# Optimization experiments

Measured on AMD Instinct MI355X. Metric: run time of the kernel, lower is better.

The kernel has to match this reference:

```python
import jax, jax.numpy as jnp
import numpy as np

EMB = 512
GP = 128
NH = 8
HD = EMB // NH  # 64
B = 2
S = 1024


def _rel_shift(x):
    # Faithful port of DoubleAttentionLayer._rel_shift (pads dim 1, reinterprets
    # (B, J+1, K, n) as (J+1, B, K, n), drops first slice). Row-major reshape
    # semantics match torch .view on contiguous tensors exactly.
    Bsz, J, K, N = x.shape
    zp = jnp.zeros((Bsz, 1, K, N), x.dtype)
    xp = jnp.concatenate([zp, x], axis=1).reshape(J + 1, Bsz, K, N)
    return xp[1:].reshape(Bsz, J, K, N)


def _layernorm(x):
    # nn.LayerNorm(emb_dim, elementwise_affine=False), eps=1e-5
    m = jnp.mean(x, axis=-1, keepdims=True)
    v = jnp.var(x, axis=-1, keepdims=True)
    return (x - m) / jnp.sqrt(v + 1e-5)


def _attention(q, k, v, Bc, Bp, gpe, mask, Wp_w, Wp_b):
    Bsz, J, E = q.shape
    K = k.shape[1]
    # content scores
    qc = jnp.tanh((q + Bc).reshape(Bsz, J, NH, HD))
    kh = jnp.tanh(k.reshape(Bsz, K, NH, HD))
    ctx = jnp.einsum('bjnd,bknd->bjkn', qc, kh)
    # position scores (tanh before reshape in source for qp -- elementwise, same math)
    qp = jnp.tanh(q + Bp).reshape(Bsz, J, NH, HD)
    kp = jnp.tanh((gpe @ Wp_w + Wp_b).reshape(Bsz, -1, NH, HD))
    pos = jnp.einsum('bjnd,bknd->bjkn', qp, kp)
    pad = ctx.shape[2] - pos.shape[2]  # static; 0 in this configuration
    if pad > 0:
        # replicate-pad pos at front of k dim; constant(0)-pad mask (torch F.pad defaults)
        pos = jnp.concatenate([jnp.broadcast_to(pos[:, :, :1], (Bsz, J, pad, NH)), pos], axis=2)
        mask = jnp.concatenate([jnp.zeros(mask.shape[:2] + (pad, mask.shape[3]), mask.dtype), mask], axis=2)
    pos = _rel_shift(pos)
    att = (ctx + pos) / (HD ** 0.5) - 1e30 * mask
    att = jax.nn.softmax(att, axis=2)
    vh = jnp.tanh(v.reshape(Bsz, K, NH, HD))
    return jnp.einsum('bjkn,bknd->bjnd', att, vh).reshape(Bsz, J, E)


def setup_inputs() -> dict:
    key = jax.random.key(0)
    ks = jax.random.split(key, 12)
    u_emb = jax.random.normal(ks[0], (B, S, EMB), jnp.float32)
    f_emb = jax.random.normal(ks[1], (B, S, EMB), jnp.float32)
    gpe = jax.random.normal(ks[2], (B, S, GP), jnp.float32)
    # causal masks: 1 where attention is disallowed, broadcast over heads
    causal = (1.0 - jnp.tril(jnp.ones((S, S), jnp.float32)))[None, :, :, None]
    u_mask = jnp.broadcast_to(causal, (B, S, S, 1))
    f_mask = jnp.broadcast_to(causal, (B, S, S, 1))
    w = 0.02
    Wq_w = w * jax.random.normal(ks[3], (EMB, EMB), jnp.float32)
    Wq_b = jnp.zeros((EMB,), jnp.float32)
    Wkv_w = w * jax.random.normal(ks[4], (EMB, 2 * EMB), jnp.float32)
    Wkv_b = jnp.zeros((2 * EMB,), jnp.float32)
    Wp_w = w * jax.random.normal(ks[5], (GP, EMB), jnp.float32)
    Wp_b = jnp.zeros((EMB,), jnp.float32)
    Wu_w = w * jax.random.normal(ks[6], (EMB, EMB), jnp.float32)
    Wu_b = jnp.zeros((EMB,), jnp.float32)
    Bfc = 0.2 * jax.random.normal(ks[7], (1, 1, EMB), jnp.float32)
    Bfp = 0.2 * jax.random.normal(ks[8], (1, 1, EMB), jnp.float32)
    Buc = 0.2 * jax.random.normal(ks[9], (1, 1, EMB), jnp.float32)
    Bup = 0.2 * jax.random.normal(ks[10], (1, 1, EMB), jnp.float32)
    return {"u_emb": u_emb, "f_emb": f_emb, "gpe": gpe, "u_mask": u_mask, "f_mask": f_mask,
            "Wq_w": Wq_w, "Wq_b": Wq_b, "Wkv_w": Wkv_w, "Wkv_b": Wkv_b,
            "Wp_w": Wp_w, "Wp_b": Wp_b, "Wu_w": Wu_w, "Wu_b": Wu_b,
            "Bfc": Bfc, "Bfp": Bfp, "Buc": Buc, "Bup": Bup}


def reference(u_emb, f_emb, gpe, u_mask, f_mask, Wq_w, Wq_b, Wkv_w, Wkv_b,
              Wp_w, Wp_b, Wu_w, Wu_b, Bfc, Bfp, Buc, Bup):
    # first_part=True path: f_mem = f_emb (memory buffer registration has no output effect)
    q_u = f_emb @ Wu_w + Wu_b
    kv = f_emb @ Wkv_w + Wkv_b
    k, v = jnp.split(kv, 2, axis=-1)
    u_out = _layernorm(u_emb + _attention(q_u, k, v, Buc, Bup, gpe, u_mask, Wp_w, Wp_b))
    # last_layer=False: second attention over f stream
    q_f = f_emb @ Wq_w + Wq_b
    f_out = _layernorm(f_emb + _attention(q_f, k, v, Bfc, Bfp, gpe, f_mask, Wp_w, Wp_b))
    return (u_out, f_out)
```

## Files before the change

kernel.cpp:

```cpp
#include <hip/hip_runtime.h>
#include <math.h>

#define EMB 512
#define NH 8
#define HD 64
#define BB 2
#define SS 1024
#define ROWS (BB * SS)

typedef __attribute__((ext_vector_type(8))) short bhalf8;
typedef __attribute__((ext_vector_type(4))) float f32x4;
typedef __attribute__((ext_vector_type(8))) unsigned short us8;
typedef unsigned short ushort_t;

typedef const __attribute__((address_space(1))) void gas_void;
typedef __attribute__((address_space(3))) void las_void;

__device__ __forceinline__ void gl2lds16(const void* g, void* l) {
  __builtin_amdgcn_global_load_lds((gas_void*)g, (las_void*)l, 16, 0, 0);
}

__device__ __forceinline__ unsigned short f2bf(float x) {
  unsigned u = __float_as_uint(x);
  u = (u + 0x7FFFu + ((u >> 16) & 1u)) >> 16;
  return (unsigned short)u;
}
__device__ __forceinline__ float bf2f(unsigned short v) {
  return __uint_as_float(((unsigned)v) << 16);
}
__device__ __forceinline__ float fast_tanh(float x) {
  x = fminf(15.f, fmaxf(-15.f, x));
  const float e = __expf(2.f * x);
  return (e - 1.f) / (e + 1.f);
}

__global__ __launch_bounds__(256) void prep_kernel(
    const float* __restrict__ f_emb, const float* __restrict__ gpe,
    const float* __restrict__ Wu, const float* __restrict__ Wq,
    const float* __restrict__ Wkv, const float* __restrict__ Wp,
    ushort_t* __restrict__ fembB, ushort_t* __restrict__ gpeB,
    ushort_t* __restrict__ WuT, ushort_t* __restrict__ WqT,
    ushort_t* __restrict__ WkvT, ushort_t* __restrict__ WpT,
    ushort_t* __restrict__ Qcomb) {
  __shared__ __align__(16) ushort_t sT[64 * 72];
  const int bid = blockIdx.x;
  const int tid = threadIdx.x;

  if (bid < 160) {
    const bool isF = bid < 128;
    const float* src = isF ? f_emb : gpe;
    ushort_t* dst = isF ? fembB : gpeB;
    const size_t base = (size_t)(isF ? bid : bid - 128) * 8192;
#pragma unroll
    for (int j = 0; j < 4; ++j) {
      const size_t off = base + ((size_t)j * 256 + tid) * 8;
      const float4 a = *(const float4*)&src[off];
      const float4 b = *(const float4*)&src[off + 4];
      us8 o;
      o[0] = f2bf(a.x); o[1] = f2bf(a.y); o[2] = f2bf(a.z); o[3] = f2bf(a.w);
      o[4] = f2bf(b.x); o[5] = f2bf(b.y); o[6] = f2bf(b.z); o[7] = f2bf(b.w);
      *(us8*)&dst[off] = o;
    }
  } else if (bid < 432) {
    int t = bid - 160;
    const float* W;
    ushort_t* WT;
    int Nw, Kd, k0, n0;
    if (t < 64) {
      W = Wu; WT = WuT; Nw = 512; Kd = 512;
      k0 = (t >> 3) * 64; n0 = (t & 7) * 64;
    } else if (t < 128) {
      t -= 64; W = Wq; WT = WqT; Nw = 512; Kd = 512;
      k0 = (t >> 3) * 64; n0 = (t & 7) * 64;
    } else if (t < 256) {
      t -= 128; W = Wkv; WT = WkvT; Nw = 1024; Kd = 512;
      k0 = (t >> 4) * 64; n0 = (t & 15) * 64;
    } else {
      t -= 256; W = Wp; WT = WpT; Nw = 512; Kd = 128;
      k0 = (t >> 3) * 64; n0 = (t & 7) * 64;
    }
    const int kk = tid >> 2, seg = tid & 3;
    const float* src = &W[(size_t)(k0 + kk) * Nw + n0 + seg * 16];
    float v[16];
    *(float4*)&v[0] = *(const float4*)&src[0];
    *(float4*)&v[4] = *(const float4*)&src[4];
    *(float4*)&v[8] = *(const float4*)&src[8];
    *(float4*)&v[12] = *(const float4*)&src[12];
#pragma unroll
    for (int i = 0; i < 16; ++i) sT[(seg * 16 + i) * 72 + kk] = f2bf(v[i]);
    __syncthreads();
#pragma unroll
    for (int p = 0; p < 2; ++p) {
      const int idx = p * 256 + tid;
      const int n = idx >> 3, c8 = (idx & 7) * 8;
      const us8 o = *(const us8*)&sT[n * 72 + c8];
      *(us8*)&WT[(size_t)(n0 + n) * Kd + k0 + c8] = o;
    }
  } else {
    const int t2 = tid >> 7, rem = tid & 127;
    const int h = rem >> 4, d4 = (rem & 15) * 4;
    *(ushort4*)&Qcomb[((size_t)t2 * ROWS + 1023) * 1024 + h * 128 + 64 + d4] =
        make_ushort4(0, 0, 0, 0);
  }
}

__global__ __launch_bounds__(256, 3) void projpe_kernel(
    const ushort_t* __restrict__ fembB, const ushort_t* __restrict__ gpeB,
    const ushort_t* __restrict__ WuT, const ushort_t* __restrict__ WqT,
    const ushort_t* __restrict__ WkvT, const ushort_t* __restrict__ WpT,
    const float* __restrict__ Wu_b, const float* __restrict__ Wq_b,
    const float* __restrict__ Wkv_b, const float* __restrict__ Wp_b,
    const float* __restrict__ Buc, const float* __restrict__ Bup,
    const float* __restrict__ Bfc, const float* __restrict__ Bfp,
    ushort_t* __restrict__ Qcomb, ushort_t* __restrict__ Kcomb,
    ushort_t* __restrict__ vhT) {
  const int bx = blockIdx.x;
  const int mb = blockIdx.y * 128;
  const int tid = threadIdx.x;
  const int w = tid >> 6, lane = tid & 63;
  const int ln = lane & 15, quad = lane >> 4;
  const int wm = (w >> 1) * 64, wn = (w & 1) * 32;

  __shared__ __align__(16) ushort_t sMem[24576];

  const bool isPe = (bx >= 32);
  const int nb = isPe ? 0 : bx * 64;
  const int npbase = isPe ? (bx - 32) * 64 : 0;
  const ushort_t* Asrc = isPe ? gpeB : fembB;
  const int lda = isPe ? 128 : 512;
  const int trips = isPe ? 2 : 8;

  const ushort_t* Wt;
  int Kd, coff;
  if (isPe) { Wt = WpT; Kd = 128; coff = npbase; }
  else if (nb < 512) { Wt = WuT; Kd = 512; coff = nb; }
  else if (nb < 1024) { Wt = WqT; Kd = 512; coff = nb - 512; }
  else { Wt = WkvT; Kd = 512; coff = nb - 1024; }

  const int l3 = lane >> 3, c7 = lane & 7;
  const int swz = (c7 ^ l3) * 8;

#define STAGE_PP(T_, P_)                                                     \
  {                                                                          \
    const int k1_ = (T_) * 64;                                               \
    ushort_t* dA_ = sMem + (P_) * 8192;                                      \
    ushort_t* dB_ = sMem + 16384 + (P_) * 4096;                              \
    _Pragma("unroll") for (int s_ = 0; s_ < 4; ++s_) {                       \
      const int q_ = w * 4 + s_;                                             \
      const int r_ = q_ * 8 + l3;                                            \
      gl2lds16(&Asrc[(size_t)(mb + r_) * lda + k1_ + swz], &dA_[q_ * 512]);  \
    }                                                                        \
    _Pragma("unroll") for (int s_ = 0; s_ < 2; ++s_) {                       \
      const int q_ = w * 2 + s_;                                             \
      const int r_ = q_ * 8 + l3;                                            \
      gl2lds16(&Wt[(size_t)(coff + r_) * Kd + k1_ + swz], &dB_[q_ * 512]);   \
    }                                                                        \
  }

  f32x4 acc[4][2];
#pragma unroll
  for (int rt = 0; rt < 4; ++rt)
#pragma unroll
    for (int ct = 0; ct < 2; ++ct) acc[rt][ct] = (f32x4){0.f, 0.f, 0.f, 0.f};

  STAGE_PP(0, 0);

  for (int t0 = 0; t0 < trips; ++t0) {
    __syncthreads();
    if (t0 < trips - 1) STAGE_PP(t0 + 1, (t0 + 1) & 1);
    const ushort_t* bA = sMem + (t0 & 1) * 8192;
    const ushort_t* bB = sMem + 16384 + (t0 & 1) * 4096;
#pragma unroll
    for (int kc = 0; kc < 2; ++kc) {
      bhalf8 af[4], bfr[2];
#pragma unroll
      for (int rt = 0; rt < 4; ++rt) {
        const int row = wm + rt * 16 + ln;
        af[rt] = *(const bhalf8*)&bA[row * 64 +
                                     (((kc * 4 + quad) ^ (row & 7)) << 3)];
      }
#pragma unroll
      for (int ct = 0; ct < 2; ++ct) {
        const int row = wn + ct * 16 + ln;
        bfr[ct] = *(const bhalf8*)&bB[row * 64 +
                                      (((kc * 4 + quad) ^ (row & 7)) << 3)];
      }
#pragma unroll
      for (int rt = 0; rt < 4; ++rt)
#pragma unroll
        for (int ct = 0; ct < 2; ++ct)
          acc[rt][ct] = __builtin_amdgcn_mfma_f32_16x16x32_bf16(
              af[rt], bfr[ct], acc[rt][ct], 0, 0, 0);
    }
  }

  __syncthreads();
  ushort_t* sOut = sMem;

  if (!isPe && nb >= 1536) {
#pragma unroll
    for (int ct = 0; ct < 2; ++ct) {
      const int nl = wn + ct * 16 + ln;
      const float wb = Wkv_b[nb + nl - 1024];
#pragma unroll
      for (int rt = 0; rt < 4; ++rt)
#pragma unroll
        for (int r = 0; r < 4; ++r) {
          const int ml = wm + rt * 16 + quad * 4 + r;
          sOut[nl * 136 + ml] = f2bf(fast_tanh(acc[rt][ct][r] + wb));
        }
    }
    __syncthreads();
    const int b = mb >> 10, mo = mb & 1023;
#pragma unroll
    for (int i = 0; i < 4; ++i) {
      const int idx = tid + i * 256;
      const int nl = idx >> 4, m8 = (idx & 15) * 8;
      const us8 v = *(const us8*)&sOut[nl * 136 + m8];
      *(us8*)&vhT[((size_t)b * 512 + (nb - 1536) + nl) * 1024 + mo + m8] = v;
    }
  } else {
    const float* WB =
        isPe ? Wp_b : (nb < 512 ? Wu_b : (nb < 1024 ? Wq_b : Wkv_b));
    const int woff =
        isPe ? npbase : (nb < 512 ? nb : (nb < 1024 ? nb - 512 : nb - 1024));
    const bool rawDump = (!isPe && nb < 1024);
#pragma unroll
    for (int ct = 0; ct < 2; ++ct) {
      const int nl = wn + ct * 16 + ln;
      const float wb = WB[woff + nl];
#pragma unroll
      for (int rt = 0; rt < 4; ++rt)
#pragma unroll
        for (int r = 0; r < 4; ++r) {
          const int ml = wm + rt * 16 + quad * 4 + r;
          const float v = acc[rt][ct][r] + wb;
          sOut[ml * 72 + nl] = f2bf(rawDump ? v : fast_tanh(v));
        }
    }
    __syncthreads();
#pragma unroll
    for (int i = 0; i < 4; ++i) {
      const int idx = tid + i * 256;
      const int rr = idx >> 3, c8 = (idx & 7) * 8;
      const int m = mb + rr;
      const us8 v = *(const us8*)&sOut[rr * 72 + c8];
      if (isPe) {
        const int n = npbase + c8;
        const int h = n >> 6;
        *(us8*)&Kcomb[(size_t)m * 1024 + h * 128 + 64 + (n & 63)] = v;
      } else if (nb < 1024) {
        const int strm = nb >= 512 ? 1 : 0;
        const int n = (nb - strm * 512) + c8;
        const int h = n >> 6;
        const float* BC = strm ? Bfc : Buc;
        const float* BP = strm ? Bfp : Bup;
        float bcA[8], bpA[8];
        *(float4*)&bcA[0] = *(const float4*)&BC[n];
        *(float4*)&bcA[4] = *(const float4*)&BC[n + 4];
        *(float4*)&bpA[0] = *(const float4*)&BP[n];
        *(float4*)&bpA[4] = *(const float4*)&BP[n + 4];
        us8 oc, op;
#pragma unroll
        for (int jj = 0; jj < 8; ++jj) {
          const float vv = bf2f((unsigned short)v[jj]);
          oc[jj] = f2bf(fast_tanh(vv + bcA[jj]));
          op[jj] = f2bf(fast_tanh(vv + bpA[jj]));
        }
        *(us8*)&Qcomb[((size_t)strm * ROWS + m) * 1024 + h * 128 + (n & 63)] =
            oc;
        if (m != 0) {
          const int mp = (m < 1024) ? m - 1 : m;
          *(us8*)&Qcomb[((size_t)strm * ROWS + mp) * 1024 + h * 128 + 64 +
                        (n & 63)] = op;
        }
      } else {
        const int n = (nb - 1024) + c8;
        const int h = n >> 6;
        *(us8*)&Kcomb[(size_t)m * 1024 + h * 128 + (n & 63)] = v;
      }
    }
  }
}

__global__ __launch_bounds__(512, 2) void attn_kernel(
    const ushort_t* __restrict__ Qcomb, const ushort_t* __restrict__ Kcomb,
    const ushort_t* __restrict__ vhT, float* __restrict__ Ofin) {
  const int bid = blockIdx.x;
  const int tid = threadIdx.x;
  const int w = tid >> 6, lane = tid & 63;
  const int ln = lane & 15, quad = lane >> 4;
  const int wr = w >> 1, wc = w & 1;
  const int l4 = lane >> 4, p15 = lane & 15;
  const int l3 = lane >> 3, l7 = lane & 7;

  __shared__ __align__(16) ushort_t sK[2 * 8192];
  __shared__ __align__(16) ushort_t sV[2 * 4096];
  __shared__ __align__(16) ushort_t sP[64 * 72];
  __shared__ float lsf[2][64];

  const int c = bid >> 3, pi = bid & 7;
  const int jA = 15 - pi, jB = pi;
  const int t = c >> 4, b = (c >> 3) & 1, h = c & 7;

#define STAGE_KV(KT_, BUF_)                                                   \
  {                                                                           \
    const size_t kb_ = ((size_t)b * SS + (KT_)*64) * 1024 + h * 128;          \
    ushort_t* bk_ = sK + (BUF_)*8192;                                         \
    _Pragma("unroll") for (int s_ = 0; s_ < 2; ++s_) {                        \
      const int q_ = w * 2 + s_;                                              \
      const int r_ = q_ * 4 + l4;                                             \
      const int gl_ = p15 ^ (r_ & 7);                                         \
      gl2lds16(&Kcomb[kb_ + (size_t)r_ * 1024 + gl_ * 8], &bk_[q_ * 512]);    \
    }                                                                         \
    const size_t vb_ = ((size_t)b * 512 + h * 64) * 1024 + (KT_)*64;          \
    ushort_t* bv_ = sV + (BUF_)*4096;                                         \
    {                                                                         \
      const int r_ = w * 8 + l3;                                              \
      const int gl_ = l7 ^ (r_ & 7);                                          \
      gl2lds16(&vhT[vb_ + (size_t)r_ * 1024 + gl_ * 8], &bv_[w * 512]);       \
    }                                                                         \
  }

  bhalf8 aq[4];
#define LOAD_AQ(JT_)                                                          \
  {                                                                           \
    const size_t qb_ =                                                        \
        ((size_t)t * ROWS + b * SS + (JT_)*64 + wr * 16 + ln) * 1024 +        \
        h * 128 + quad * 8;                                                   \
    _Pragma("unroll") for (int kc_ = 0; kc_ < 4; ++kc_) aq[kc_] =             \
        *(const bhalf8*)&Qcomb[qb_ + kc_ * 32];                               \
  }

  STAGE_KV(0, 0);
  LOAD_AQ(jA);

  f32x4 oacc[2];
  oacc[0] = (f32x4){0.f, 0.f, 0.f, 0.f};
  oacc[1] = (f32x4){0.f, 0.f, 0.f, 0.f};
  float lsum[4] = {0.f, 0.f, 0.f, 0.f};

  int jt = jA, kt = 0;
  for (int it = 0; it < 17; ++it) {
    __syncthreads();
    const ushort_t* bK = sK + (it & 1) * 8192;
    const ushort_t* bV = sV + (it & 1) * 4096;

    int jt2 = jt, kt2 = kt + 1;
    if (kt2 > jt) { jt2 = jB; kt2 = 0; }
    if (it < 16) STAGE_KV(kt2, ((it + 1) & 1));

    f32x4 sacc[2];
#pragma unroll
    for (int ct = 0; ct < 2; ++ct) {
      sacc[ct] = (f32x4){0.f, 0.f, 0.f, 0.f};
#pragma unroll
      for (int kc = 0; kc < 4; ++kc) {
        const bhalf8 bk =
            *(const bhalf8*)&bK[(wc * 32 + ct * 16 + ln) * 128 +
                                (((kc * 4 + quad) ^ l7) << 3)];
        sacc[ct] = __builtin_amdgcn_mfma_f32_16x16x32_bf16(aq[kc], bk,
                                                           sacc[ct], 0, 0, 0);
      }
    }

    const bool diag = (kt == jt);
#pragma unroll
    for (int ct = 0; ct < 2; ++ct)
#pragma unroll
      for (int r = 0; r < 4; ++r) {
        float p;
        if (diag && (wc * 32 + ct * 16 + ln > wr * 16 + quad * 4 + r))
          p = 0.f;
        else
          p = __expf(sacc[ct][r] * 0.125f - 16.f);
        sacc[ct][r] = p;
        lsum[r] += p;
      }

#pragma unroll
    for (int ct = 0; ct < 2; ++ct)
#pragma unroll
      for (int r = 0; r < 4; ++r)
        sP[(wr * 16 + quad * 4 + r) * 72 + wc * 32 + ct * 16 + ln] =
            (ushort_t)(__float_as_uint(sacc[ct][r]) >> 16);

    asm volatile("s_waitcnt lgkmcnt(0)" ::: "memory");
    __builtin_amdgcn_s_barrier();
    __builtin_amdgcn_sched_barrier(0);

#pragma unroll
    for (int kc = 0; kc < 2; ++kc) {
      const bhalf8 ap =
          *(const bhalf8*)&sP[(wr * 16 + ln) * 72 + kc * 32 + quad * 8];
#pragma unroll
      for (int ct = 0; ct < 2; ++ct) {
        const bhalf8 bv =
            *(const bhalf8*)&bV[(wc * 32 + ct * 16 + ln) * 64 +
                                (((kc * 4 + quad) ^ l7) << 3)];
        oacc[ct] = __builtin_amdgcn_mfma_f32_16x16x32_bf16(ap, bv, oacc[ct],
                                                           0, 0, 0);
      }
    }

    if (kt == jt) {
#pragma unroll
      for (int r = 0; r < 4; ++r) {
        float s = lsum[r];
        s += __shfl_xor(s, 1);
        s += __shfl_xor(s, 2);
        s += __shfl_xor(s, 4);
        s += __shfl_xor(s, 8);
        if (ln == 0) lsf[wc][wr * 16 + quad * 4 + r] = s;
      }
      __syncthreads();
#pragma unroll
      for (int r = 0; r < 4; ++r) {
        const int rl = wr * 16 + quad * 4 + r;
        const float rinv = 1.f / (lsf[0][rl] + lsf[1][rl]);
        const int j = jt * 64 + rl;
        const size_t orow = (((size_t)t * ROWS + b * SS + j) << 9) + h * 64;
#pragma unroll
        for (int ct = 0; ct < 2; ++ct)
          Ofin[orow + wc * 32 + ct * 16 + ln] = oacc[ct][r] * rinv;
        lsum[r] = 0.f;
      }
      oacc[0] = (f32x4){0.f, 0.f, 0.f, 0.f};
      oacc[1] = (f32x4){0.f, 0.f, 0.f, 0.f};
      if (jt == jA) LOAD_AQ(jB);
    }
    jt = jt2; kt = kt2;
  }
}

__global__ __launch_bounds__(256) void ln_kernel(
    const float* __restrict__ u_emb, const float* __restrict__ f_emb,
    const float* __restrict__ Ofin, float* __restrict__ out) {
  const int rid = blockIdx.x * 4 + (threadIdx.x >> 6);
  const int lane = threadIdx.x & 63;
  const int t = rid >> 11, row = rid & 2047;
  const float* resid = t ? f_emb : u_emb;
  const size_t base = (size_t)row * 512;
  const size_t obase = ((size_t)t * ROWS + row) * 512;
  const int o = lane * 8;

  const float4 n0 = *(const float4*)&Ofin[obase + o];
  const float4 n1 = *(const float4*)&Ofin[obase + o + 4];
  const float4 r0 = *(const float4*)&resid[base + o];
  const float4 r1 = *(const float4*)&resid[base + o + 4];
  float y[8];
  y[0] = r0.x + n0.x; y[1] = r0.y + n0.y;
  y[2] = r0.z + n0.z; y[3] = r0.w + n0.w;
  y[4] = r1.x + n1.x; y[5] = r1.y + n1.y;
  y[6] = r1.z + n1.z; y[7] = r1.w + n1.w;

  float s = 0.f, q = 0.f;
#pragma unroll
  for (int i = 0; i < 8; ++i) {
    s += y[i];
    q += y[i] * y[i];
  }
#pragma unroll
  for (int off = 1; off < 64; off <<= 1) {
    s += __shfl_xor(s, off);
    q += __shfl_xor(q, off);
  }
  const float mean = s * (1.f / 512.f);
  const float var = q * (1.f / 512.f) - mean * mean;
  const float rstd = rsqrtf(var + 1e-5f);

  float4 o0, o1;
  o0.x = (y[0] - mean) * rstd; o0.y = (y[1] - mean) * rstd;
  o0.z = (y[2] - mean) * rstd; o0.w = (y[3] - mean) * rstd;
  o1.x = (y[4] - mean) * rstd; o1.y = (y[5] - mean) * rstd;
  o1.z = (y[6] - mean) * rstd; o1.w = (y[7] - mean) * rstd;
  *(float4*)&out[obase + o] = o0;
  *(float4*)&out[obase + o + 4] = o1;
}

extern "C" void kernel_launch(void* const* d_in, const int* in_sizes, int n_in,
                              void* d_out, int out_size, void* d_ws,
                              size_t ws_size, hipStream_t stream) {
  (void)in_sizes; (void)n_in; (void)out_size; (void)ws_size;
  const float* u_emb = (const float*)d_in[0];
  const float* f_emb = (const float*)d_in[1];
  const float* gpe = (const float*)d_in[2];
  const float* Wq_w = (const float*)d_in[5];
  const float* Wq_b = (const float*)d_in[6];
  const float* Wkv_w = (const float*)d_in[7];
  const float* Wkv_b = (const float*)d_in[8];
  const float* Wp_w = (const float*)d_in[9];
  const float* Wp_b = (const float*)d_in[10];
  const float* Wu_w = (const float*)d_in[11];
  const float* Wu_b = (const float*)d_in[12];
  const float* Bfc = (const float*)d_in[13];
  const float* Bfp = (const float*)d_in[14];
  const float* Buc = (const float*)d_in[15];
  const float* Bup = (const float*)d_in[16];
  float* out = (float*)d_out;

  ushort_t* ws = (ushort_t*)d_ws;
  const size_t SZ = (size_t)ROWS * EMB;
  ushort_t* Qcomb = ws;
  ushort_t* Kcomb = ws + 4 * SZ;
  ushort_t* vhT = ws + 6 * SZ;
  float* Ofin = (float*)(ws + 7 * SZ);
  ushort_t* fembB = ws + 12 * SZ;
  ushort_t* gpeB = ws + 13 * SZ;
  ushort_t* WuT = ws + 13 * SZ + SZ / 4;
  ushort_t* WqT = ws + 13 * SZ + SZ / 2;
  ushort_t* WkvT = ws + 13 * SZ + 3 * (SZ / 4);
  ushort_t* WpT = ws + 13 * SZ + 5 * (SZ / 4);

  dim3 blk(256);
  hipLaunchKernelGGL(prep_kernel, dim3(433), blk, 0, stream, f_emb, gpe, Wu_w,
                     Wq_w, Wkv_w, Wp_w, fembB, gpeB, WuT, WqT, WkvT, WpT,
                     Qcomb);
  hipLaunchKernelGGL(projpe_kernel, dim3(40, 16), blk, 0, stream, fembB, gpeB,
                     WuT, WqT, WkvT, WpT, Wu_b, Wq_b, Wkv_b, Wp_b, Buc, Bup,
                     Bfc, Bfp, Qcomb, Kcomb, vhT);
  hipLaunchKernelGGL(attn_kernel, dim3(256), dim3(512), 0, stream, Qcomb,
                     Kcomb, vhT, Ofin);
  hipLaunchKernelGGL(ln_kernel, dim3(1024), blk, 0, stream, u_emb, f_emb,
                     Ofin, out);
}
```

Baseline: 148.2 us.

## Give each attention block one query tile with four full-width waves

```diff
diff --git a/kernel.cpp b/kernel.cpp
--- a/kernel.cpp
+++ b/kernel.cpp
@@ -283,82 +283,74 @@
   }
 }
 
-__global__ __launch_bounds__(512, 2) void attn_kernel(
+__global__ __launch_bounds__(256, 2) void attn_kernel(
     const ushort_t* __restrict__ Qcomb, const ushort_t* __restrict__ Kcomb,
     const ushort_t* __restrict__ vhT, float* __restrict__ Ofin) {
-  const int bid = blockIdx.x;
+  const int pbid = blockIdx.x;
+  const int lbid = (pbid & 7) * 64 + (pbid >> 3);
+  const int c = lbid >> 4, jt = lbid & 15;
   const int tid = threadIdx.x;
   const int w = tid >> 6, lane = tid & 63;
   const int ln = lane & 15, quad = lane >> 4;
-  const int wr = w >> 1, wc = w & 1;
   const int l4 = lane >> 4, p15 = lane & 15;
   const int l3 = lane >> 3, l7 = lane & 7;
+  const int t = c >> 4, b = (c >> 3) & 1, h = c & 7;
 
   __shared__ __align__(16) ushort_t sK[2 * 8192];
   __shared__ __align__(16) ushort_t sV[2 * 4096];
   __shared__ __align__(16) ushort_t sP[64 * 72];
-  __shared__ float lsf[2][64];
-
-  const int c = bid >> 3, pi = bid & 7;
-  const int jA = 15 - pi, jB = pi;
-  const int t = c >> 4, b = (c >> 3) & 1, h = c & 7;
 
 #define STAGE_KV(KT_, BUF_)                                                   \
   {                                                                           \
     const size_t kb_ = ((size_t)b * SS + (KT_)*64) * 1024 + h * 128;          \
     ushort_t* bk_ = sK + (BUF_)*8192;                                         \
-    _Pragma("unroll") for (int s_ = 0; s_ < 2; ++s_) {                        \
-      const int q_ = w * 2 + s_;                                              \
+    _Pragma("unroll") for (int s_ = 0; s_ < 4; ++s_) {                        \
+      const int q_ = w * 4 + s_;                                              \
       const int r_ = q_ * 4 + l4;                                             \
       const int gl_ = p15 ^ (r_ & 7);                                         \
       gl2lds16(&Kcomb[kb_ + (size_t)r_ * 1024 + gl_ * 8], &bk_[q_ * 512]);    \
     }                                                                         \
     const size_t vb_ = ((size_t)b * 512 + h * 64) * 1024 + (KT_)*64;          \
     ushort_t* bv_ = sV + (BUF_)*4096;                                         \
-    {                                                                         \
-      const int r_ = w * 8 + l3;                                              \
+    _Pragma("unroll") for (int s_ = 0; s_ < 2; ++s_) {                        \
+      const int q_ = w * 2 + s_;                                              \
+      const int r_ = q_ * 8 + l3;                                             \
       const int gl_ = l7 ^ (r_ & 7);                                          \
-      gl2lds16(&vhT[vb_ + (size_t)r_ * 1024 + gl_ * 8], &bv_[w * 512]);       \
+      gl2lds16(&vhT[vb_ + (size_t)r_ * 1024 + gl_ * 8], &bv_[q_ * 512]);      \
     }                                                                         \
   }
 
+  STAGE_KV(0, 0);
+
   bhalf8 aq[4];
-#define LOAD_AQ(JT_)                                                          \
-  {                                                                           \
-    const size_t qb_ =                                                        \
-        ((size_t)t * ROWS + b * SS + (JT_)*64 + wr * 16 + ln) * 1024 +        \
-        h * 128 + quad * 8;                                                   \
-    _Pragma("unroll") for (int kc_ = 0; kc_ < 4; ++kc_) aq[kc_] =             \
-        *(const bhalf8*)&Qcomb[qb_ + kc_ * 32];                               \
-  }
-
-  STAGE_KV(0, 0);
-  LOAD_AQ(jA);
-
-  f32x4 oacc[2];
-  oacc[0] = (f32x4){0.f, 0.f, 0.f, 0.f};
-  oacc[1] = (f32x4){0.f, 0.f, 0.f, 0.f};
+  {
+    const size_t qb_ =
+        ((size_t)t * ROWS + b * SS + jt * 64 + w * 16 + ln) * 1024 + h * 128 +
+        quad * 8;
+#pragma unroll
+    for (int kc = 0; kc < 4; ++kc)
+      aq[kc] = *(const bhalf8*)&Qcomb[qb_ + kc * 32];
+  }
+
+  f32x4 oacc[4];
+#pragma unroll
+  for (int ct = 0; ct < 4; ++ct) oacc[ct] = (f32x4){0.f, 0.f, 0.f, 0.f};
   float lsum[4] = {0.f, 0.f, 0.f, 0.f};
 
-  int jt = jA, kt = 0;
-  for (int it = 0; it < 17; ++it) {
+  for (int kt = 0; kt <= jt; ++kt) {
     __syncthreads();
-    const ushort_t* bK = sK + (it & 1) * 8192;
-    const ushort_t* bV = sV + (it & 1) * 4096;
-
-    int jt2 = jt, kt2 = kt + 1;
-    if (kt2 > jt) { jt2 = jB; kt2 = 0; }
-    if (it < 16) STAGE_KV(kt2, ((it + 1) & 1));
-
-    f32x4 sacc[2];
-#pragma unroll
-    for (int ct = 0; ct < 2; ++ct) {
+    const ushort_t* bK = sK + (kt & 1) * 8192;
+    const ushort_t* bV = sV + (kt & 1) * 4096;
+    if (kt < jt) STAGE_KV(kt + 1, (kt + 1) & 1);
+
+    f32x4 sacc[4];
+#pragma unroll
+    for (int ct = 0; ct < 4; ++ct) {
       sacc[ct] = (f32x4){0.f, 0.f, 0.f, 0.f};
 #pragma unroll
       for (int kc = 0; kc < 4; ++kc) {
-        const bhalf8 bk =
-            *(const bhalf8*)&bK[(wc * 32 + ct * 16 + ln) * 128 +
-                                (((kc * 4 + quad) ^ l7) << 3)];
+        const bhalf8 bk = *(const bhalf8*)&bK[(ct * 16 + ln) * 128 +
+                                              (((kc * 4 + quad) ^ l7) << 3)];
         sacc[ct] = __builtin_amdgcn_mfma_f32_16x16x32_bf16(aq[kc], bk,
                                                            sacc[ct], 0, 0, 0);
       }
@@ -366,11 +358,11 @@
 
     const bool diag = (kt == jt);
 #pragma unroll
-    for (int ct = 0; ct < 2; ++ct)
+    for (int ct = 0; ct < 4; ++ct)
 #pragma unroll
       for (int r = 0; r < 4; ++r) {
         float p;
-        if (diag && (wc * 32 + ct * 16 + ln > wr * 16 + quad * 4 + r))
+        if (diag && (ct * 16 + ln > w * 16 + quad * 4 + r))
           p = 0.f;
         else
           p = __expf(sacc[ct][r] * 0.125f - 16.f);
@@ -379,57 +371,42 @@
       }
 
 #pragma unroll
-    for (int ct = 0; ct < 2; ++ct)
+    for (int ct = 0; ct < 4; ++ct)
 #pragma unroll
       for (int r = 0; r < 4; ++r)
-        sP[(wr * 16 + quad * 4 + r) * 72 + wc * 32 + ct * 16 + ln] =
+        sP[(w * 16 + quad * 4 + r) * 72 + ct * 16 + ln] =
             (ushort_t)(__float_as_uint(sacc[ct][r]) >> 16);
 
     asm volatile("s_waitcnt lgkmcnt(0)" ::: "memory");
-    __builtin_amdgcn_s_barrier();
     __builtin_amdgcn_sched_barrier(0);
 
 #pragma unroll
     for (int kc = 0; kc < 2; ++kc) {
       const bhalf8 ap =
-          *(const bhalf8*)&sP[(wr * 16 + ln) * 72 + kc * 32 + quad * 8];
-#pragma unroll
-      for (int ct = 0; ct < 2; ++ct) {
-        const bhalf8 bv =
-            *(const bhalf8*)&bV[(wc * 32 + ct * 16 + ln) * 64 +
-                                (((kc * 4 + quad) ^ l7) << 3)];
+          *(const bhalf8*)&sP[(w * 16 + ln) * 72 + kc * 32 + quad * 8];
+#pragma unroll
+      for (int ct = 0; ct < 4; ++ct) {
+        const bhalf8 bv = *(const bhalf8*)&bV[(ct * 16 + ln) * 64 +
+                                              (((kc * 4 + quad) ^ l7) << 3)];
         oacc[ct] = __builtin_amdgcn_mfma_f32_16x16x32_bf16(ap, bv, oacc[ct],
                                                            0, 0, 0);
       }
     }
-
-    if (kt == jt) {
-#pragma unroll
-      for (int r = 0; r < 4; ++r) {
-        float s = lsum[r];
-        s += __shfl_xor(s, 1);
-        s += __shfl_xor(s, 2);
-        s += __shfl_xor(s, 4);
-        s += __shfl_xor(s, 8);
-        if (ln == 0) lsf[wc][wr * 16 + quad * 4 + r] = s;
-      }
-      __syncthreads();
-#pragma unroll
-      for (int r = 0; r < 4; ++r) {
-        const int rl = wr * 16 + quad * 4 + r;
-        const float rinv = 1.f / (lsf[0][rl] + lsf[1][rl]);
-        const int j = jt * 64 + rl;
-        const size_t orow = (((size_t)t * ROWS + b * SS + j) << 9) + h * 64;
-#pragma unroll
-        for (int ct = 0; ct < 2; ++ct)
-          Ofin[orow + wc * 32 + ct * 16 + ln] = oacc[ct][r] * rinv;
-        lsum[r] = 0.f;
-      }
-      oacc[0] = (f32x4){0.f, 0.f, 0.f, 0.f};
-      oacc[1] = (f32x4){0.f, 0.f, 0.f, 0.f};
-      if (jt == jA) LOAD_AQ(jB);
-    }
-    jt = jt2; kt = kt2;
+  }
+
+#pragma unroll
+  for (int r = 0; r < 4; ++r) {
+    float s = lsum[r];
+    s += __shfl_xor(s, 1);
+    s += __shfl_xor(s, 2);
+    s += __shfl_xor(s, 4);
+    s += __shfl_xor(s, 8);
+    const float rinv = 1.f / s;
+    const int j = jt * 64 + w * 16 + quad * 4 + r;
+    const size_t orow = (((size_t)t * ROWS + b * SS + j) << 9) + h * 64;
+#pragma unroll
+    for (int ct = 0; ct < 4; ++ct)
+      Ofin[orow + ct * 16 + ln] = oacc[ct][r] * rinv;
   }
 }
 
@@ -519,8 +496,8 @@
   hipLaunchKernelGGL(projpe_kernel, dim3(40, 16), blk, 0, stream, fembB, gpeB,
                      WuT, WqT, WkvT, WpT, Wu_b, Wq_b, Wkv_b, Wp_b, Buc, Bup,
                      Bfc, Bfp, Qcomb, Kcomb, vhT);
-  hipLaunchKernelGGL(attn_kernel, dim3(256), dim3(512), 0, stream, Qcomb,
-                     Kcomb, vhT, Ofin);
+  hipLaunchKernelGGL(attn_kernel, dim3(512), blk, 0, stream, Qcomb, Kcomb,
+                     vhT, Ofin);
   hipLaunchKernelGGL(ln_kernel, dim3(1024), blk, 0, stream, u_emb, f_emb,
                      Ofin, out);
 }
```

Result: no change. 146.7 us (-1.0%).
